# Kernel optimization log

Measured on AMD Instinct MI355X. Metric: run time of the kernel, lower is better.

The kernel has to match this reference:

```python
import jax, jax.numpy as jnp
import numpy as np

KMEANS_ITERS = 10  # fixed Lloyd iterations replacing scipy kmeans (data-dependent convergence)
EPS = 1e-12


def _l2_normalize(x):
    return x / jnp.clip(jnp.linalg.norm(x, axis=-1, keepdims=True), EPS, None)


def _kmeans_labels(xn, K):
    """Lloyd k-means with deterministic evenly-spaced init. xn: (P, D) L2-normalized."""
    P = xn.shape[0]
    init_idx = jnp.arange(K) * (P // K)
    c0 = xn[init_idx]                                    # (K, D)
    x2 = jnp.sum(xn * xn, axis=-1, keepdims=True)        # (P, 1)

    def assign(c):
        # squared euclidean distances (P, K)
        d2 = x2 - 2.0 * (xn @ c.T) + jnp.sum(c * c, axis=-1)[None, :]
        return jnp.argmin(d2, axis=-1)

    def body(i, c):
        lab = assign(c)
        sums = jax.ops.segment_sum(xn, lab, num_segments=K)
        cnt = jax.ops.segment_sum(jnp.ones((P,), xn.dtype), lab, num_segments=K)
        return jnp.where(cnt[:, None] > 0, sums / jnp.maximum(cnt, 1.0)[:, None], c)

    c = jax.lax.fori_loop(0, KMEANS_ITERS, body, c0)
    return assign(c)


def _pool_one(x, K):
    """x: (P, D) -> pooled (K, D), mask (K,)."""
    xn = _l2_normalize(x)
    lab = jax.lax.stop_gradient(_kmeans_labels(jax.lax.stop_gradient(xn), K))
    P = xn.shape[0]
    sums = jax.ops.segment_sum(xn, lab, num_segments=K)
    cnt = jax.ops.segment_sum(jnp.ones((P,), xn.dtype), lab, num_segments=K)
    mean = sums / jnp.maximum(cnt, 1.0)[:, None]
    pooled = _l2_normalize(mean)
    nonempty = cnt > 0
    pooled = jnp.where(nonempty[:, None], pooled, 0.0)
    return pooled, nonempty.astype(x.dtype)


def setup_inputs() -> dict:
    key = jax.random.key(0)
    k1, = jax.random.split(key, 1)
    B, S, D = 16, 4096, 128
    hidden_states = jax.random.normal(k1, (B, S, D), dtype=jnp.float32)
    attention_mask = jnp.ones((B, S), dtype=jnp.float32)
    # all pages share the same vision-patch range [0, 3583]
    patch_range_list = jnp.tile(jnp.array([[0, 3583]], dtype=jnp.int64), (B, 1))
    return {
        "hidden_states": hidden_states,
        "attention_mask": attention_mask,
        "patch_range_list": patch_range_list,
        "merge_size": 4,
    }


def reference(hidden_states, attention_mask, patch_range_list, merge_size):
    B, S, D = hidden_states.shape
    r0 = int(patch_range_list[0, 0])
    r1 = int(patch_range_list[0, 1])
    vision_end_token_index = r1 + 1
    P = r1 - r0 + 1
    K = max(P // merge_size, 1)                       # max_clusters
    max_tokens = -(-S // merge_size)                  # ceil(S / merge_size)

    hidden_states_tail = hidden_states[:, vision_end_token_index + 1:-1]  # (B, T, D)
    tail_len = hidden_states_tail.shape[1]

    patch_embeds = hidden_states[:, r0:r1 + 1]        # (B, P, D)
    pooled, mask = jax.vmap(lambda x: _pool_one(x, K))(patch_embeds)  # (B,K,D), (B,K)

    new_hidden_states = jnp.zeros((B, max_tokens, D), dtype=hidden_states.dtype)
    new_hidden_states = new_hidden_states.at[:, max_tokens - K:].set(pooled)
    new_attention_mask = jnp.zeros((B, max_tokens), dtype=hidden_states.dtype)
    new_attention_mask = new_attention_mask.at[:, max_tokens - K:].set(mask)

    new_hidden_states = jnp.concatenate([new_hidden_states, hidden_states_tail], axis=1)
    new_attention_mask = jnp.concatenate(
        [new_attention_mask, jnp.ones((B, tail_len), dtype=hidden_states.dtype)], axis=1)
    return new_hidden_states, new_attention_mask
```

## Files before the change

kernel.cpp:

```cpp
#include <hip/hip_runtime.h>
#include <math.h>

#define B_  16
#define S_  4096
#define D_  128
#define R0_ 0
#define R1_ 3583
#define P_  3584
#define MERGE_ 4
#define K_  896
#define MAXTOK_ 1024
#define PAD_ 128
#define TAILSTART_ 3585
#define TAILLEN_ 510
#define TOK_ 1534
#define ITERS_ 10
#define EPS_ 1e-12f

#define NG_ 56

typedef short bf16x8 __attribute__((ext_vector_type(8)));
typedef float f32x4 __attribute__((ext_vector_type(4)));

__device__ __forceinline__ unsigned short f2bh(float f) {
  unsigned u = __float_as_uint(f);
  unsigned r = u + 0x7fffu + ((u >> 16) & 1u);
  return (unsigned short)(r >> 16);
}
__device__ __forceinline__ float bh2f(unsigned short h) {
  return __uint_as_float(((unsigned)h) << 16);
}

__device__ __forceinline__ void split3(const float* v, bf16x8& h, bf16x8& m, bf16x8& l) {
#pragma unroll
  for (int i = 0; i < 8; ++i) {
    unsigned short hh = f2bh(v[i]); float r1 = v[i] - bh2f(hh);
    unsigned short mm = f2bh(r1);   float r2 = r1 - bh2f(mm);
    unsigned short ll = f2bh(r2);
    h[i] = (short)hh; m[i] = (short)mm; l[i] = (short)ll;
  }
}

__global__ __launch_bounds__(256) void normalize_kernel(const float* __restrict__ hs,
                                                        float* __restrict__ xn) {
  int row = blockIdx.x * 4 + (threadIdx.x >> 6);
  int lane = threadIdx.x & 63;
  if (row >= B_ * P_) return;
  int b = row / P_, p = row % P_;
  float2 v = *reinterpret_cast<const float2*>(hs + ((size_t)b * S_ + R0_ + p) * D_ + lane * 2);
  float ss = v.x * v.x + v.y * v.y;
#pragma unroll
  for (int off = 32; off; off >>= 1) ss += __shfl_xor(ss, off);
  float denom = fmaxf(sqrtf(ss), EPS_);
  float2 nv; nv.x = v.x / denom; nv.y = v.y / denom;
  *reinterpret_cast<float2*>(xn + (size_t)row * D_ + lane * 2) = nv;
}

__global__ __launch_bounds__(256) void init_cent_kernel(const float* __restrict__ xn,
                                                        float* __restrict__ c,
                                                        float* __restrict__ c2) {
  int w = blockIdx.x * 4 + (threadIdx.x >> 6);
  int lane = threadIdx.x & 63;
  if (w >= B_ * K_) return;
  int b = w / K_, k = w % K_;
  float2 v = *reinterpret_cast<const float2*>(xn + ((size_t)b * P_ + k * MERGE_) * D_ + lane * 2);
  *reinterpret_cast<float2*>(c + ((size_t)w) * D_ + lane * 2) = v;
  float ss = v.x * v.x + v.y * v.y;
#pragma unroll
  for (int off = 32; off; off >>= 1) ss += __shfl_xor(ss, off);
  if (lane == 0) c2[w] = ss;
}

__global__ __launch_bounds__(256) void pack_B_kernel(const float* __restrict__ cc,
                                                     const float* __restrict__ c2,
                                                     bf16x8* __restrict__ bp,
                                                     float* __restrict__ c2p) {
  int job = blockIdx.x * 4 + (threadIdx.x >> 6);
  int lane = threadIdx.x & 63;
  if (job >= B_ * NG_ * 4) return;
  int b = job / (NG_ * 4);
  int rem = job % (NG_ * 4);
  int g = rem >> 2, s = rem & 3;
  int col = g * 16 + (lane & 15);
  int d0 = s * 32 + (lane >> 4) * 8;
  const float* src = cc + ((size_t)b * K_ + col) * D_ + d0;
  float v[8];
  *reinterpret_cast<float4*>(&v[0]) = *reinterpret_cast<const float4*>(src);
  *reinterpret_cast<float4*>(&v[4]) = *reinterpret_cast<const float4*>(src + 4);
  bf16x8 h, m, l;
  split3(v, h, m, l);
  size_t base = (size_t)b * (NG_ * 4 * 3 * 64) + (size_t)((g * 4 + s) * 3) * 64;
  bp[base + lane] = h;
  bp[base + 64 + lane] = m;
  bp[base + 128 + lane] = l;
  if (s == 0) c2p[((size_t)b * NG_ + g) * 64 + lane] = c2[b * K_ + col];
}

__global__ __launch_bounds__(128, 2) void assign_mfma_kernel(const float* __restrict__ xn,
                                                             const bf16x8* __restrict__ bp,
                                                             const float* __restrict__ c2p,
                                                             int* __restrict__ labels,
                                                             int* __restrict__ cnt) {
  int bid = blockIdx.x;
  int xcd = bid & 7;
  int idx = bid >> 3;
  int b = 2 * xcd + (idx >= 56 ? 1 : 0);
  int mb = (idx >= 56) ? idx - 56 : idx;
  int tid = threadIdx.x;
  int widx = tid >> 6, lane = tid & 63;
  int l15 = lane & 15, lg = lane >> 4;
  int base_row = mb * 64 + widx * 32;

  bf16x8 fa[2][4][3];
  {
    const float* xb = xn + (size_t)b * P_ * D_;
#pragma unroll
    for (int mi = 0; mi < 2; ++mi)
#pragma unroll
      for (int s = 0; s < 4; ++s) {
        const float* src = xb + (size_t)(base_row + mi * 16 + l15) * D_ + s * 32 + lg * 8;
        float v[8];
        *reinterpret_cast<float4*>(&v[0]) = *reinterpret_cast<const float4*>(src);
        *reinterpret_cast<float4*>(&v[4]) = *reinterpret_cast<const float4*>(src + 4);
        split3(v, fa[mi][s][0], fa[mi][s][1], fa[mi][s][2]);
      }
  }

  float bestd[8]; int bestk[8];
#pragma unroll
  for (int i = 0; i < 8; ++i) { bestd[i] = 3.4e38f; bestk[i] = 0; }

  const bf16x8* bpb = bp + (size_t)b * (NG_ * 4 * 3 * 64);
  const float* c2b = c2p + (size_t)b * (NG_ * 64);

#define MFMA_(A, Bf, C) __builtin_amdgcn_mfma_f32_16x16x32_bf16(A, Bf, C, 0, 0, 0)
#define SIX(accv, mi, s, FB)                      \
  accv = MFMA_(fa[mi][s][0], FB[s][0], accv);     \
  accv = MFMA_(fa[mi][s][0], FB[s][1], accv);     \
  accv = MFMA_(fa[mi][s][1], FB[s][0], accv);     \
  accv = MFMA_(fa[mi][s][0], FB[s][2], accv);     \
  accv = MFMA_(fa[mi][s][2], FB[s][0], accv);     \
  accv = MFMA_(fa[mi][s][1], FB[s][1], accv);

#define LOADFB(FB, C2V, G) do {                                            \
    int g_ = (G);                                                          \
    for (int s_ = 0; s_ < 4; ++s_)                                         \
      for (int t_ = 0; t_ < 3; ++t_)                                       \
        FB[s_][t_] = bpb[(size_t)((g_ * 4 + s_) * 3 + t_) * 64 + lane];    \
    C2V = c2b[g_ * 64 + lane];                                             \
  } while (0)

#define COMPUTE(FB, C2V, G) do {                                           \
    f32x4 a00 = {0.f,0.f,0.f,0.f}, a01 = {0.f,0.f,0.f,0.f};                \
    f32x4 a10 = {0.f,0.f,0.f,0.f}, a11 = {0.f,0.f,0.f,0.f};                \
    SIX(a00, 0, 0, FB) SIX(a10, 1, 0, FB) SIX(a01, 0, 2, FB) SIX(a11, 1, 2, FB) \
    SIX(a00, 0, 1, FB) SIX(a10, 1, 1, FB) SIX(a01, 0, 3, FB) SIX(a11, 1, 3, FB) \
    int kcol = (G) * 16 + l15;                                             \
    for (int r_ = 0; r_ < 4; ++r_) {                                       \
      float d0v = fmaf(-2.f, a00[r_] + a01[r_], C2V);                      \
      if (d0v < bestd[r_]) { bestd[r_] = d0v; bestk[r_] = kcol; }          \
      float d1v = fmaf(-2.f, a10[r_] + a11[r_], C2V);                      \
      if (d1v < bestd[4 + r_]) { bestd[4 + r_] = d1v; bestk[4 + r_] = kcol; } \
    }                                                                      \
  } while (0)

  bf16x8 fbA[4][3], fbB[4][3];
  float c2A, c2B;
  LOADFB(fbA, c2A, 0);
  for (int g = 0; g < NG_; g += 2) {
    LOADFB(fbB, c2B, g + 1);
    COMPUTE(fbA, c2A, g);
    int gn = (g + 2 < NG_) ? g + 2 : 0;
    LOADFB(fbA, c2A, gn);
    COMPUTE(fbB, c2B, g + 1);
  }
#undef COMPUTE
#undef LOADFB
#undef SIX
#undef MFMA_

#pragma unroll
  for (int slot = 0; slot < 8; ++slot) {
    float bd = bestd[slot]; int bk = bestk[slot];
#pragma unroll
    for (int off = 8; off; off >>= 1) {
      float od = __shfl_down(bd, off, 16);
      int   ok = __shfl_down(bk, off, 16);
      if (od < bd || (od == bd && ok < bk)) { bd = od; bk = ok; }
    }
    if (l15 == 0) {
      int mi = slot >> 2, r = slot & 3;
      int row = base_row + mi * 16 + 4 * lg + r;
      labels[(size_t)b * P_ + row] = bk;
      atomicAdd(&cnt[b * K_ + bk], 1);
    }
  }
}

__global__ __launch_bounds__(1024) void scan_scatter_kernel(const int* __restrict__ cnt,
                                                            const int* __restrict__ labels,
                                                            int* __restrict__ starts,
                                                            int* __restrict__ order) {
  __shared__ int sm[1024];
  __shared__ int cur[K_];
  int b = blockIdx.x, t = threadIdx.x;
  int v = (t < K_) ? cnt[b * K_ + t] : 0;
  sm[t] = v;
  __syncthreads();
  for (int off = 1; off < 1024; off <<= 1) {
    int u = (t >= off) ? sm[t - off] : 0;
    __syncthreads();
    sm[t] += u;
    __syncthreads();
  }
  if (t < K_) { int ex = sm[t] - v; starts[b * K_ + t] = ex; cur[t] = ex; }
  __syncthreads();
#pragma unroll
  for (int r = 0; r < (P_ + 1023) / 1024; ++r) {
    int p = r * 1024 + t;
    if (p < P_) {
      int lab = labels[b * P_ + p];
      int pos = atomicAdd(&cur[lab], 1);
      order[b * P_ + pos] = p;
    }
  }
}

__global__ __launch_bounds__(256) void update_kernel(const float* __restrict__ xn,
                                                     const int* __restrict__ order,
                                                     const int* __restrict__ cnt,
                                                     const int* __restrict__ starts,
                                                     float* __restrict__ c,
                                                     float* __restrict__ c2) {
  int w = blockIdx.x * 4 + (threadIdx.x >> 6);
  int lane = threadIdx.x & 63;
  if (w >= B_ * K_) return;
  int b = w / K_;
  int n = cnt[w], st = starts[w];
  const float* xb = xn + (size_t)b * P_ * D_;
  float2 acc = make_float2(0.f, 0.f);
  for (int i = 0; i < n; ++i) {
    int p = order[b * P_ + st + i];
    float2 v = *reinterpret_cast<const float2*>(xb + (size_t)p * D_ + lane * 2);
    acc.x += v.x; acc.y += v.y;
  }
  float* cp = c + (size_t)w * D_ + lane * 2;
  float2 cur;
  if (n > 0) {
    float dn = (float)n;
    cur.x = acc.x / dn; cur.y = acc.y / dn;
    *reinterpret_cast<float2*>(cp) = cur;
  } else {
    cur = *reinterpret_cast<const float2*>(cp);
  }
  float ss = cur.x * cur.x + cur.y * cur.y;
#pragma unroll
  for (int off = 32; off; off >>= 1) ss += __shfl_xor(ss, off);
  if (lane == 0) c2[w] = ss;
}

__global__ __launch_bounds__(256) void pool_kernel(const float* __restrict__ xn,
                                                   const int* __restrict__ order,
                                                   const int* __restrict__ cnt,
                                                   const int* __restrict__ starts,
                                                   float* __restrict__ outh,
                                                   float* __restrict__ outm) {
  int w = blockIdx.x * 4 + (threadIdx.x >> 6);
  int lane = threadIdx.x & 63;
  if (w >= B_ * K_) return;
  int b = w / K_, k = w % K_;
  int n = cnt[w], st = starts[w];
  const float* xb = xn + (size_t)b * P_ * D_;
  float2 acc = make_float2(0.f, 0.f);
  for (int i = 0; i < n; ++i) {
    int p = order[b * P_ + st + i];
    float2 v = *reinterpret_cast<const float2*>(xb + (size_t)p * D_ + lane * 2);
    acc.x += v.x; acc.y += v.y;
  }
  float dn = (float)(n > 0 ? n : 1);
  float2 mean; mean.x = acc.x / dn; mean.y = acc.y / dn;
  float ss = mean.x * mean.x + mean.y * mean.y;
#pragma unroll
  for (int off = 32; off; off >>= 1) ss += __shfl_xor(ss, off);
  float denom = fmaxf(sqrtf(ss), EPS_);
  float2 pv;
  if (n > 0) { pv.x = mean.x / denom; pv.y = mean.y / denom; }
  else       { pv.x = 0.f; pv.y = 0.f; }
  int tok = PAD_ + k;
  *reinterpret_cast<float2*>(outh + ((size_t)b * TOK_ + tok) * D_ + lane * 2) = pv;
  if (lane == 0) outm[b * TOK_ + tok] = (n > 0) ? 1.f : 0.f;
}

__global__ __launch_bounds__(256) void assemble_kernel(const float* __restrict__ hs,
                                                       float* __restrict__ outh,
                                                       float* __restrict__ outm) {
  const int ROWS = PAD_ + TAILLEN_;
  int w = blockIdx.x * 4 + (threadIdx.x >> 6);
  int lane = threadIdx.x & 63;
  if (w >= B_ * ROWS) return;
  int b = w / ROWS, r = w % ROWS;
  int tok; float2 v; float m;
  if (r < PAD_) {
    tok = r; v = make_float2(0.f, 0.f); m = 0.f;
  } else {
    tok = MAXTOK_ + (r - PAD_);
    v = *reinterpret_cast<const float2*>(hs + ((size_t)b * S_ + TAILSTART_ + (r - PAD_)) * D_ + lane * 2);
    m = 1.f;
  }
  *reinterpret_cast<float2*>(outh + ((size_t)b * TOK_ + tok) * D_ + lane * 2) = v;
  if (lane == 0) outm[b * TOK_ + tok] = m;
}

extern "C" void kernel_launch(void* const* d_in, const int* in_sizes, int n_in,
                              void* d_out, int out_size, void* d_ws, size_t ws_size,
                              hipStream_t stream) {
  const float* hs = (const float*)d_in[0];
  float* outh = (float*)d_out;
  float* outm = outh + (size_t)B_ * TOK_ * D_;

  char* wsb = (char*)d_ws;
  size_t off = 0;
  auto alloc = [&](size_t bytes) -> void* {
    void* p = wsb + off;
    off += (bytes + 255) & ~(size_t)255;
    return p;
  };
  float*  xn     = (float*) alloc((size_t)B_ * P_ * D_ * sizeof(float));
  float*  cc     = (float*) alloc((size_t)B_ * K_ * D_ * sizeof(float));
  bf16x8* bpack  = (bf16x8*)alloc((size_t)B_ * NG_ * 4 * 3 * 64 * 16);
  float*  c2     = (float*) alloc((size_t)B_ * K_ * sizeof(float));
  float*  c2p    = (float*) alloc((size_t)B_ * NG_ * 64 * sizeof(float));
  int*    labels = (int*)   alloc((size_t)B_ * P_ * sizeof(int));
  int*    cnt    = (int*)   alloc((size_t)B_ * K_ * sizeof(int));
  int*    starts = (int*)   alloc((size_t)B_ * K_ * sizeof(int));
  int*    order  = (int*)   alloc((size_t)B_ * P_ * sizeof(int));
  (void)ws_size; (void)in_sizes; (void)n_in; (void)out_size;

  normalize_kernel<<<(B_ * P_ + 3) / 4, 256, 0, stream>>>(hs, xn);
  init_cent_kernel<<<(B_ * K_ + 3) / 4, 256, 0, stream>>>(xn, cc, c2);
  pack_B_kernel<<<B_ * NG_, 256, 0, stream>>>(cc, c2, bpack, c2p);

  for (int it = 0; it < ITERS_; ++it) {
    hipMemsetAsync(cnt, 0, (size_t)B_ * K_ * sizeof(int), stream);
    assign_mfma_kernel<<<896, 128, 0, stream>>>(xn, bpack, c2p, labels, cnt);
    scan_scatter_kernel<<<B_, 1024, 0, stream>>>(cnt, labels, starts, order);
    update_kernel<<<(B_ * K_ + 3) / 4, 256, 0, stream>>>(xn, order, cnt, starts, cc, c2);
    pack_B_kernel<<<B_ * NG_, 256, 0, stream>>>(cc, c2, bpack, c2p);
  }

  hipMemsetAsync(cnt, 0, (size_t)B_ * K_ * sizeof(int), stream);
  assign_mfma_kernel<<<896, 128, 0, stream>>>(xn, bpack, c2p, labels, cnt);
  scan_scatter_kernel<<<B_, 1024, 0, stream>>>(cnt, labels, starts, order);
  pool_kernel<<<(B_ * K_ + 3) / 4, 256, 0, stream>>>(xn, order, cnt, starts, outh, outm);
  assemble_kernel<<<(B_ * (PAD_ + TAILLEN_) + 3) / 4, 256, 0, stream>>>(hs, outh, outm);
}
```

Before: 1.175 ms.

## Split assign kernel over centroid halves with merge pass and deterministic scatter

Splits the centroid dimension of the assignment kernel into two halves, doubling the grid to 1792 blocks so more work is in flight per device. Each half writes partial best distance and index, and a new merge kernel picks the winner, writes labels and does the count atomics. The scatter step now ranks equal labels within a wavefront using shuffles and serialises wavefronts with barriers, which makes the ordering deterministic. The c2 repacking is dropped and c2 is read directly. The cost is an extra launch, extra partial-result traffic, and A-fragment split work repeated per half.

```diff
diff --git a/kernel.cpp b/kernel.cpp
--- a/kernel.cpp
+++ b/kernel.cpp
@@ -18,6 +18,8 @@
 #define EPS_ 1e-12f
 
 #define NG_ 56
+#define NGH_ 28
+#define BP_ (B_ * P_)
 
 typedef short bf16x8 __attribute__((ext_vector_type(8)));
 typedef float f32x4 __attribute__((ext_vector_type(4)));
@@ -72,9 +74,7 @@
 }
 
 __global__ __launch_bounds__(256) void pack_B_kernel(const float* __restrict__ cc,
-                                                     const float* __restrict__ c2,
-                                                     bf16x8* __restrict__ bp,
-                                                     float* __restrict__ c2p) {
+                                                     bf16x8* __restrict__ bp) {
   int job = blockIdx.x * 4 + (threadIdx.x >> 6);
   int lane = threadIdx.x & 63;
   if (job >= B_ * NG_ * 4) return;
@@ -93,19 +93,21 @@
   bp[base + lane] = h;
   bp[base + 64 + lane] = m;
   bp[base + 128 + lane] = l;
-  if (s == 0) c2p[((size_t)b * NG_ + g) * 64 + lane] = c2[b * K_ + col];
 }
 
 __global__ __launch_bounds__(128, 2) void assign_mfma_kernel(const float* __restrict__ xn,
                                                              const bf16x8* __restrict__ bp,
-                                                             const float* __restrict__ c2p,
-                                                             int* __restrict__ labels,
-                                                             int* __restrict__ cnt) {
+                                                             const float* __restrict__ c2,
+                                                             float* __restrict__ pd,
+                                                             int* __restrict__ pk) {
   int bid = blockIdx.x;
   int xcd = bid & 7;
   int idx = bid >> 3;
-  int b = 2 * xcd + (idx >= 56 ? 1 : 0);
-  int mb = (idx >= 56) ? idx - 56 : idx;
+  int b = 2 * xcd + (idx >= 112 ? 1 : 0);
+  int inner = (idx >= 112) ? idx - 112 : idx;
+  int mb = inner >> 1;
+  int kh = inner & 1;
+  int g0 = kh * NGH_;
   int tid = threadIdx.x;
   int widx = tid >> 6, lane = tid & 63;
   int l15 = lane & 15, lg = lane >> 4;
@@ -131,7 +133,7 @@
   for (int i = 0; i < 8; ++i) { bestd[i] = 3.4e38f; bestk[i] = 0; }
 
   const bf16x8* bpb = bp + (size_t)b * (NG_ * 4 * 3 * 64);
-  const float* c2b = c2p + (size_t)b * (NG_ * 64);
+  const float* c2b = c2 + (size_t)b * K_;
 
 #define MFMA_(A, Bf, C) __builtin_amdgcn_mfma_f32_16x16x32_bf16(A, Bf, C, 0, 0, 0)
 #define SIX(accv, mi, s, FB)                      \
@@ -147,7 +149,7 @@
     for (int s_ = 0; s_ < 4; ++s_)                                         \
       for (int t_ = 0; t_ < 3; ++t_)                                       \
         FB[s_][t_] = bpb[(size_t)((g_ * 4 + s_) * 3 + t_) * 64 + lane];    \
-    C2V = c2b[g_ * 64 + lane];                                             \
+    C2V = c2b[g_ * 16 + l15];                                              \
   } while (0)
 
 #define COMPUTE(FB, C2V, G) do {                                           \
@@ -166,11 +168,11 @@
 
   bf16x8 fbA[4][3], fbB[4][3];
   float c2A, c2B;
-  LOADFB(fbA, c2A, 0);
-  for (int g = 0; g < NG_; g += 2) {
+  LOADFB(fbA, c2A, g0);
+  for (int g = g0; g < g0 + NGH_; g += 2) {
     LOADFB(fbB, c2B, g + 1);
     COMPUTE(fbA, c2A, g);
-    int gn = (g + 2 < NG_) ? g + 2 : 0;
+    int gn = (g + 2 < g0 + NGH_) ? g + 2 : g0;
     LOADFB(fbA, c2A, gn);
     COMPUTE(fbB, c2B, g + 1);
   }
@@ -191,10 +193,24 @@
     if (l15 == 0) {
       int mi = slot >> 2, r = slot & 3;
       int row = base_row + mi * 16 + 4 * lg + r;
-      labels[(size_t)b * P_ + row] = bk;
-      atomicAdd(&cnt[b * K_ + bk], 1);
+      size_t o = (size_t)kh * BP_ + (size_t)b * P_ + row;
+      pd[o] = bd;
+      pk[o] = bk;
     }
   }
+}
+
+__global__ __launch_bounds__(256) void merge_kernel(const float* __restrict__ pd,
+                                                    const int* __restrict__ pk,
+                                                    int* __restrict__ labels,
+                                                    int* __restrict__ cnt) {
+  int i = blockIdx.x * 256 + threadIdx.x;
+  if (i >= BP_) return;
+  float d0 = pd[i], d1 = pd[BP_ + i];
+  int k = (d1 < d0) ? pk[BP_ + i] : pk[i];
+  labels[i] = k;
+  int b = i / P_;
+  atomicAdd(&cnt[b * K_ + k], 1);
 }
 
 __global__ __launch_bounds__(1024) void scan_scatter_kernel(const int* __restrict__ cnt,
@@ -204,6 +220,7 @@
   __shared__ int sm[1024];
   __shared__ int cur[K_];
   int b = blockIdx.x, t = threadIdx.x;
+  int lane = t & 63, widx = t >> 6;
   int v = (t < K_) ? cnt[b * K_ + t] : 0;
   sm[t] = v;
   __syncthreads();
@@ -215,13 +232,23 @@
   }
   if (t < K_) { int ex = sm[t] - v; starts[b * K_ + t] = ex; cur[t] = ex; }
   __syncthreads();
-#pragma unroll
-  for (int r = 0; r < (P_ + 1023) / 1024; ++r) {
+
+  for (int r = 0; r < 4; ++r) {
     int p = r * 1024 + t;
-    if (p < P_) {
-      int lab = labels[b * P_ + p];
-      int pos = atomicAdd(&cur[lab], 1);
-      order[b * P_ + pos] = p;
+    bool valid = (p < P_);
+    int lab = valid ? labels[b * P_ + p] : -1;
+    int rank = 0, tot = 0;
+    for (int j = 0; j < 64; ++j) {
+      int labj = __shfl(lab, j);
+      if (labj == lab) { tot++; if (j < lane) rank++; }
+    }
+    for (int w = 0; w < 16; ++w) {
+      if (widx == w && valid) {
+        int base = cur[lab];
+        order[b * P_ + base + rank] = p;
+        if (rank == tot - 1) cur[lab] = base + tot;
+      }
+      __syncthreads();
     }
   }
 }
@@ -329,27 +356,30 @@
   float*  cc     = (float*) alloc((size_t)B_ * K_ * D_ * sizeof(float));
   bf16x8* bpack  = (bf16x8*)alloc((size_t)B_ * NG_ * 4 * 3 * 64 * 16);
   float*  c2     = (float*) alloc((size_t)B_ * K_ * sizeof(float));
-  float*  c2p    = (float*) alloc((size_t)B_ * NG_ * 64 * sizeof(float));
-  int*    labels = (int*)   alloc((size_t)B_ * P_ * sizeof(int));
+  float*  pd     = (float*) alloc((size_t)2 * BP_ * sizeof(float));
+  int*    pk     = (int*)   alloc((size_t)2 * BP_ * sizeof(int));
+  int*    labels = (int*)   alloc((size_t)BP_ * sizeof(int));
   int*    cnt    = (int*)   alloc((size_t)B_ * K_ * sizeof(int));
   int*    starts = (int*)   alloc((size_t)B_ * K_ * sizeof(int));
-  int*    order  = (int*)   alloc((size_t)B_ * P_ * sizeof(int));
+  int*    order  = (int*)   alloc((size_t)BP_ * sizeof(int));
   (void)ws_size; (void)in_sizes; (void)n_in; (void)out_size;
 
   normalize_kernel<<<(B_ * P_ + 3) / 4, 256, 0, stream>>>(hs, xn);
   init_cent_kernel<<<(B_ * K_ + 3) / 4, 256, 0, stream>>>(xn, cc, c2);
-  pack_B_kernel<<<B_ * NG_, 256, 0, stream>>>(cc, c2, bpack, c2p);
+  pack_B_kernel<<<B_ * NG_, 256, 0, stream>>>(cc, bpack);
 
   for (int it = 0; it < ITERS_; ++it) {
     hipMemsetAsync(cnt, 0, (size_t)B_ * K_ * sizeof(int), stream);
-    assign_mfma_kernel<<<896, 128, 0, stream>>>(xn, bpack, c2p, labels, cnt);
+    assign_mfma_kernel<<<1792, 128, 0, stream>>>(xn, bpack, c2, pd, pk);
+    merge_kernel<<<(BP_ + 255) / 256, 256, 0, stream>>>(pd, pk, labels, cnt);
     scan_scatter_kernel<<<B_, 1024, 0, stream>>>(cnt, labels, starts, order);
     update_kernel<<<(B_ * K_ + 3) / 4, 256, 0, stream>>>(xn, order, cnt, starts, cc, c2);
-    pack_B_kernel<<<B_ * NG_, 256, 0, stream>>>(cc, c2, bpack, c2p);
+    pack_B_kernel<<<B_ * NG_, 256, 0, stream>>>(cc, bpack);
   }
 
   hipMemsetAsync(cnt, 0, (size_t)B_ * K_ * sizeof(int), stream);
-  assign_mfma_kernel<<<896, 128, 0, stream>>>(xn, bpack, c2p, labels, cnt);
+  assign_mfma_kernel<<<1792, 128, 0, stream>>>(xn, bpack, c2, pd, pk);
+  merge_kernel<<<(BP_ + 255) / 256, 256, 0, stream>>>(pd, pk, labels, cnt);
   scan_scatter_kernel<<<B_, 1024, 0, stream>>>(cnt, labels, starts, order);
   pool_kernel<<<(B_ * K_ + 3) / 4, 256, 0, stream>>>(xn, order, cnt, starts, outh, outm);
   assemble_kernel<<<(B_ * (PAD_ + TAILLEN_) + 3) / 4, 256, 0, stream>>>(hs, outh, outm);
```

New measurement: 1.409 ms. 1.2x slower.
